# Optimization experiments

Measured on AMD Instinct MI355X. Metric: run time of the kernel, lower is better.

## Reference

```python
import jax, jax.numpy as jnp
import numpy as np

NUM_HEADS = 16
HEAD_DIM = 64
SCALE = HEAD_DIM ** -0.5


def setup_inputs() -> dict:
    key = jax.random.key(0)
    ks = jax.random.split(key, 5)
    B, N, C = 2, 2048, 1024
    x = jax.random.normal(ks[0], (B, N, C), dtype=jnp.float32)
    rel_pos_bias = jax.random.normal(ks[1], (NUM_HEADS, N, N), dtype=jnp.float32) * 0.02
    qkv_w = jax.random.normal(ks[2], (3 * C, C), dtype=jnp.float32) * (C ** -0.5)
    q_bias = jnp.zeros((C,), dtype=jnp.float32)
    v_bias = jnp.zeros((C,), dtype=jnp.float32)
    proj_w = jax.random.normal(ks[3], (C, C), dtype=jnp.float32) * (C ** -0.5)
    proj_b = jnp.zeros((C,), dtype=jnp.float32)
    return {"x": x, "rel_pos_bias": rel_pos_bias, "qkv_w": qkv_w,
            "q_bias": q_bias, "v_bias": v_bias, "proj_w": proj_w, "proj_b": proj_b}


def reference(x, rel_pos_bias, qkv_w, q_bias, v_bias, proj_w, proj_b):
    B, N, C = x.shape
    H, D = NUM_HEADS, HEAD_DIM
    # qkv bias = concat(q_bias, zeros, v_bias)
    qkv_b = jnp.concatenate([q_bias, jnp.zeros_like(v_bias), v_bias])
    qkv = x @ qkv_w.T + qkv_b                       # [B, N, 3C]
    qkv = qkv.reshape(B, N, 3, H, D).transpose(2, 0, 3, 1, 4)  # [3, B, H, N, D]
    q, k, v = qkv[0], qkv[1], qkv[2]
    q = q * SCALE
    attn = jnp.einsum('bhnd,bhmd->bhnm', q, k)      # [B, H, N, N]
    attn = attn + rel_pos_bias[None]                # bias broadcast over batch
    attn = jax.nn.softmax(attn, axis=-1)
    out = jnp.einsum('bhnm,bhmd->bhnd', attn, v)    # [B, H, N, D]
    out = out.transpose(0, 2, 1, 3).reshape(B, N, H * D)
    out = out @ proj_w.T + proj_b
    return out
```

## Files before the change

kernel.cpp:

```cpp
#include <hip/hip_runtime.h>

typedef unsigned short u16;
typedef short bfrag __attribute__((ext_vector_type(8)));
typedef float facc  __attribute__((ext_vector_type(4)));

#define LOG2E 1.44269504088896340736f

static __device__ __forceinline__ u16 f2bf(float x) {
  union { float f; unsigned u; } v; v.f = x;
  return (u16)((v.u + 0x7FFFu + ((v.u >> 16) & 1u)) >> 16);
}
static __device__ __forceinline__ void gload_lds16(const u16* g, u16* l) {
  __builtin_amdgcn_global_load_lds((const __attribute__((address_space(1))) void*)g,
                                   (__attribute__((address_space(3))) void*)l,
                                   16, 0, 0);
}
static __device__ __forceinline__ void gload_lds16f_nt(const float* g, float* l) {
  __builtin_amdgcn_global_load_lds((const __attribute__((address_space(1))) void*)g,
                                   (__attribute__((address_space(3))) void*)l,
                                   16, 0, 2);
}

__global__ __launch_bounds__(256) void convert_kernel(
    const float* __restrict__ x, const float* __restrict__ qw, const float* __restrict__ pw,
    u16* __restrict__ xb, u16* __restrict__ qwb, u16* __restrict__ pwb)
{
  const int NX = 4 * 1024 * 1024, NQ = 3 * 1024 * 1024, NP = 1024 * 1024;
  const int total4 = (NX + NQ + NP) >> 2;
  for (int i = blockIdx.x * blockDim.x + threadIdx.x; i < total4;
       i += gridDim.x * blockDim.x) {
    const int e = i << 2;
    const float* s; u16* d; int off;
    if (e < NX)            { s = x;  d = xb;  off = e; }
    else if (e < NX + NQ)  { s = qw; d = qwb; off = e - NX; }
    else                   { s = pw; d = pwb; off = e - NX - NQ; }
    float4 v = *(const float4*)(s + off);
    ushort4 o;
    o.x = f2bf(v.x); o.y = f2bf(v.y); o.z = f2bf(v.z); o.w = f2bf(v.w);
    *(ushort4*)(d + off) = o;
  }
}

static __device__ __forceinline__ void gemm128_bt(
    const u16* __restrict__ A, const u16* __restrict__ B, int K,
    int m0, int n0, u16* As, u16* Bs, facc acc[4][4])
{
  const int lane = threadIdx.x & 63;
  const int wv   = threadIdx.x >> 6;
  const int quad = lane >> 4;
  const int l15  = lane & 15;
  const int wm = wv >> 1, wn = wv & 1;
  const int srow = lane >> 2;
  const int skb  = (lane & 3) * 8;

  facc zero = {0.f, 0.f, 0.f, 0.f};
#pragma unroll
  for (int i = 0; i < 4; ++i)
#pragma unroll
    for (int j = 0; j < 4; ++j) acc[i][j] = zero;

  const int nIter = K >> 5;
  for (int kk = 0; kk < nIter; ++kk) {
    const int k0 = kk << 5;
    __syncthreads();
#pragma unroll
    for (int c = 0; c < 2; ++c) {
      const int seg = wv * 2 + c;
      gload_lds16(A + (long)(m0 + seg * 16 + srow) * K + k0 + skb, As + seg * 512);
      gload_lds16(B + (long)(n0 + seg * 16 + srow) * K + k0 + skb, Bs + seg * 512);
    }
    __syncthreads();
    bfrag af[4], bf[4];
#pragma unroll
    for (int i = 0; i < 4; ++i)
      af[i] = *(const bfrag*)(As + (wm * 64 + i * 16 + l15) * 32 + quad * 8);
#pragma unroll
    for (int j = 0; j < 4; ++j)
      bf[j] = *(const bfrag*)(Bs + (wn * 64 + j * 16 + l15) * 32 + quad * 8);
#pragma unroll
    for (int i = 0; i < 4; ++i)
#pragma unroll
      for (int j = 0; j < 4; ++j)
        acc[i][j] = __builtin_amdgcn_mfma_f32_16x16x32_bf16(af[i], bf[j], acc[i][j], 0, 0, 0);
  }
}

__global__ __launch_bounds__(256) void qkv_gemm_kernel(
    const u16* __restrict__ x, const u16* __restrict__ w,
    const float* __restrict__ qb, const float* __restrict__ vb,
    u16* __restrict__ Q, u16* __restrict__ Kd, u16* __restrict__ Vt)
{
  __shared__ u16 As[128 * 32];
  __shared__ u16 Bs[128 * 32];
  facc acc[4][4];
  const int m0 = blockIdx.y * 128;
  const int n0 = blockIdx.x * 128;
  gemm128_bt(x, w, 1024, m0, n0, As, Bs, acc);

  const int lane = threadIdx.x & 63;
  const int wv = threadIdx.x >> 6;
  const int quad = lane >> 4, l15 = lane & 15;
  const int wm = wv >> 1, wn = wv & 1;
  const int ncb = n0 + wn * 64;
  const int which = ncb >> 10;
  const int h = (ncb >> 6) & 15;

#pragma unroll
  for (int j = 0; j < 4; ++j) {
    const int d = j * 16 + l15;
    const int n_g = ncb + d;
#pragma unroll
    for (int i = 0; i < 4; ++i) {
      const int mg0 = m0 + wm * 64 + i * 16 + quad * 4;
      const int b  = mg0 >> 11;
      const int ns = mg0 & 2047;
      if (which == 0) {
        const float qbv = qb[n_g];
#pragma unroll
        for (int r = 0; r < 4; ++r)
          Q[(((long)(b * 16 + h) * 2048 + ns + r) << 6) + d] =
              f2bf((acc[i][j][r] + qbv) * 0.125f);
      } else if (which == 1) {
#pragma unroll
        for (int r = 0; r < 4; ++r)
          Kd[(((long)(b * 16 + h) * 2048 + ns + r) << 6) + d] = f2bf(acc[i][j][r]);
      } else {
        const float vbv = vb[n_g - 2048];
        ushort4 pk;
        pk.x = f2bf(acc[i][j][0] + vbv);
        pk.y = f2bf(acc[i][j][1] + vbv);
        pk.z = f2bf(acc[i][j][2] + vbv);
        pk.w = f2bf(acc[i][j][3] + vbv);
        *(ushort4*)(Vt + (((long)((b * 16 + h) * 64 + d)) << 11) + ns) = pk;
      }
    }
  }
}

__global__ __launch_bounds__(256, 8) void attn_kernel(
    const u16* __restrict__ Q, const u16* __restrict__ Kd, const u16* __restrict__ Vt,
    const float* __restrict__ bias, float* __restrict__ Part)
{
  __shared__ u16 P[4][16 * 64];
  __shared__ float BiasS[2][2][16 * 64];
  const int lane = threadIdx.x & 63;
  const int wv = threadIdx.x >> 6;
  const int quad = lane >> 4, l15 = lane & 15;
  const int L  = (blockIdx.x & 7) * 256 + (blockIdx.x >> 3);
  const int h  = L >> 7;
  const int ks = (L >> 6) & 1;
  const int qg = L & 63;
  const int q0 = qg * 32;
  const int b  = wv & 1;
  const int qh = wv >> 1;
  const int bh = b * 16 + h;
  const int qw = q0 + qh * 16;
  const int ksBase = ks << 10;
  const long baseN = (long)bh << 17;

  bfrag qf0 = *(const bfrag*)(Q + baseN + (long)(qw + l15) * 64 + quad * 8);
  bfrag qf1 = *(const bfrag*)(Q + baseN + (long)(qw + l15) * 64 + 32 + quad * 8);

  facc o[4];
  float m_i[4], l_i[4];
  facc zero = {0.f, 0.f, 0.f, 0.f};
#pragma unroll
  for (int t = 0; t < 4; ++t) o[t] = zero;
#pragma unroll
  for (int r = 0; r < 4; ++r) { m_i[r] = -1e30f; l_i[r] = 0.f; }

  const float* bh_bias = bias + ((long)h << 22) + ((long)q0 << 11);
  char* PwB = (char*)&P[wv][0];

  auto stage = [&](int buf, int kk) {
#pragma unroll
    for (int cc = 0; cc < 2; ++cc) {
      const int c_ = b * 2 + cc;
      const int row_ = c_ * 4 + quad;
      gload_lds16f_nt(bh_bias + (long)(qh * 16 + row_) * 2048 + kk
                        + ((l15 * 4) ^ ((row_ & 7) << 2)),
                      &BiasS[buf][qh][0] + c_ * 256);
    }
  };

  stage(0, ksBase);

  for (int it = 0; it < 16; ++it) {
    const int k0 = ksBase + it * 64;
    __syncthreads();

    facc s[4];
#pragma unroll
    for (int kt = 0; kt < 4; ++kt) {
      const u16* kb = Kd + baseN + (long)(k0 + kt * 16 + l15) * 64;
      bfrag kf0 = *(const bfrag*)(kb + quad * 8);
      bfrag kf1 = *(const bfrag*)(kb + 32 + quad * 8);
      facc z = zero;
      z = __builtin_amdgcn_mfma_f32_16x16x32_bf16(qf0, kf0, z, 0, 0, 0);
      z = __builtin_amdgcn_mfma_f32_16x16x32_bf16(qf1, kf1, z, 0, 0, 0);
      s[kt] = z;
    }

    const float* bs = &BiasS[it & 1][qh][0];
#pragma unroll
    for (int kt = 0; kt < 4; ++kt)
#pragma unroll
      for (int r = 0; r < 4; ++r) {
        const int row = quad * 4 + r;
        s[kt][r] += bs[row * 64 + ((kt * 16 + l15) ^ ((row & 7) << 2))];
      }

    if (it + 1 < 16) stage((it + 1) & 1, k0 + 64);

    float alpha[4];
#pragma unroll
    for (int r = 0; r < 4; ++r) {
      float v = fmaxf(fmaxf(s[0][r], s[1][r]), fmaxf(s[2][r], s[3][r]));
      v = fmaxf(v, __shfl_xor(v, 1, 16));
      v = fmaxf(v, __shfl_xor(v, 2, 16));
      v = fmaxf(v, __shfl_xor(v, 4, 16));
      v = fmaxf(v, __shfl_xor(v, 8, 16));
      const float mn = fmaxf(m_i[r], v);
      alpha[r] = exp2f((m_i[r] - mn) * LOG2E);
      m_i[r] = mn;
    }
#pragma unroll
    for (int r = 0; r < 4; ++r) {
      const float p0 = exp2f((s[0][r] - m_i[r]) * LOG2E);
      const float p1 = exp2f((s[1][r] - m_i[r]) * LOG2E);
      const float p2 = exp2f((s[2][r] - m_i[r]) * LOG2E);
      const float p3 = exp2f((s[3][r] - m_i[r]) * LOG2E);
      s[0][r] = p0; s[1][r] = p1; s[2][r] = p2; s[3][r] = p3;
      float v = (p0 + p1) + (p2 + p3);
      v += __shfl_xor(v, 1, 16);
      v += __shfl_xor(v, 2, 16);
      v += __shfl_xor(v, 4, 16);
      v += __shfl_xor(v, 8, 16);
      l_i[r] = l_i[r] * alpha[r] + v;
    }
#pragma unroll
    for (int t = 0; t < 4; ++t)
#pragma unroll
      for (int r = 0; r < 4; ++r) o[t][r] *= alpha[r];

#pragma unroll
    for (int kt = 0; kt < 4; ++kt)
#pragma unroll
      for (int r = 0; r < 4; ++r) {
        const int bo = (kt * 2 + (l15 >> 3)) * 256 + (quad * 4 + r) * 16 + (l15 & 7) * 2;
        *(u16*)(PwB + bo) = f2bf(s[kt][r]);
      }

#pragma unroll
    for (int p = 0; p < 2; ++p) {
      bfrag pfp = *(const bfrag*)(PwB + p * 1024 + lane * 16);
#pragma unroll
      for (int t = 0; t < 4; ++t) {
        bfrag vf = *(const bfrag*)(Vt + baseN + (((long)(t * 16 + l15)) << 11)
                                   + k0 + p * 32 + quad * 8);
        o[t] = __builtin_amdgcn_mfma_f32_16x16x32_bf16(pfp, vf, o[t], 0, 0, 0);
      }
    }
  }

  const long prBase = ((long)ks * 65536 + (long)bh * 2048 + qw) * 80;
#pragma unroll
  for (int t = 0; t < 4; ++t)
#pragma unroll
    for (int r = 0; r < 4; ++r)
      Part[prBase + (long)(quad * 4 + r) * 80 + t * 16 + l15] = o[t][r];
#pragma unroll
  for (int r = 0; r < 4; ++r)
    if (l15 < 2)
      Part[prBase + (long)(quad * 4 + r) * 80 + 64 + l15] = (l15 == 0) ? m_i[r] : l_i[r];
}

__global__ __launch_bounds__(256) void combine_kernel(
    const float* __restrict__ Part, u16* __restrict__ AO)
{
  const int lane = threadIdx.x & 63;
  const int wv = threadIdx.x >> 6;
  const long row = (long)blockIdx.x * 4 + wv;
  const int bh = (int)(row >> 11);
  const int q  = (int)(row & 2047);
  const int b = bh >> 4, h = bh & 15;
  const float* p0 = Part + row * 80;
  const float* p1 = Part + (row + 65536) * 80;
  const float o0 = p0[lane], o1 = p1[lane];
  const float m0 = p0[64], l0 = p0[65];
  const float m1 = p1[64], l1 = p1[65];
  const float m = fmaxf(m0, m1);
  const float w0 = exp2f((m0 - m) * LOG2E);
  const float w1 = exp2f((m1 - m) * LOG2E);
  const float ov = (o0 * w0 + o1 * w1) / (l0 * w0 + l1 * w1);
  AO[(((long)(b * 2048 + q)) << 10) + h * 64 + lane] = f2bf(ov);
}

__global__ __launch_bounds__(256) void proj_kernel(
    const u16* __restrict__ Ain, const u16* __restrict__ w,
    const float* __restrict__ pb, float* __restrict__ out)
{
  __shared__ u16 As[128 * 32];
  __shared__ u16 Bs[128 * 32];
  facc acc[4][4];
  const int m0 = blockIdx.y * 128;
  const int n0 = blockIdx.x * 128;
  gemm128_bt(Ain, w, 1024, m0, n0, As, Bs, acc);

  const int lane = threadIdx.x & 63;
  const int wv = threadIdx.x >> 6;
  const int quad = lane >> 4, l15 = lane & 15;
  const int wm = wv >> 1, wn = wv & 1;
#pragma unroll
  for (int j = 0; j < 4; ++j) {
    const int n_g = n0 + wn * 64 + j * 16 + l15;
    const float pbv = pb[n_g];
#pragma unroll
    for (int i = 0; i < 4; ++i) {
      const int mg0 = m0 + wm * 64 + i * 16 + quad * 4;
#pragma unroll
      for (int r = 0; r < 4; ++r)
        out[(((long)(mg0 + r)) << 10) + n_g] = acc[i][j][r] + pbv;
    }
  }
}

extern "C" void kernel_launch(void* const* d_in, const int* in_sizes, int n_in,
                              void* d_out, int out_size, void* d_ws, size_t ws_size,
                              hipStream_t stream)
{
  const float* x    = (const float*)d_in[0];
  const float* bias = (const float*)d_in[1];
  const float* qkvw = (const float*)d_in[2];
  const float* qb   = (const float*)d_in[3];
  const float* vb   = (const float*)d_in[4];
  const float* pw   = (const float*)d_in[5];
  const float* pb   = (const float*)d_in[6];
  float* out = (float*)d_out;

  char* ws = (char*)d_ws;
  u16* Q    = (u16*)(ws);
  u16* Kd   = (u16*)(ws + (size_t)8  * 1024 * 1024);
  u16* Vt   = (u16*)(ws + (size_t)16 * 1024 * 1024);
  u16* AO   = (u16*)(ws + (size_t)24 * 1024 * 1024);
  u16* xb   = (u16*)(ws + (size_t)32 * 1024 * 1024);
  u16* qwb  = (u16*)(ws + (size_t)40 * 1024 * 1024);
  u16* pwb  = (u16*)(ws + (size_t)46 * 1024 * 1024);
  float* Part = (float*)(ws + (size_t)48 * 1024 * 1024);

  hipLaunchKernelGGL(convert_kernel, dim3(1024), dim3(256), 0, stream,
                     x, qkvw, pw, xb, qwb, pwb);
  hipLaunchKernelGGL(qkv_gemm_kernel, dim3(24, 32), dim3(256), 0, stream,
                     xb, qwb, qb, vb, Q, Kd, Vt);
  hipLaunchKernelGGL(attn_kernel, dim3(2048), dim3(256), 0, stream,
                     Q, Kd, Vt, bias, Part);
  hipLaunchKernelGGL(combine_kernel, dim3(16384), dim3(256), 0, stream,
                     Part, AO);
  hipLaunchKernelGGL(proj_kernel, dim3(8, 32), dim3(256), 0, stream,
                     AO, pwb, pb, out);
}
```

Baseline: 656.8 us.

## Transpose MFMA operands so each lane owns one query row in attention

Swaps the A/B operands of the QK^T and PV MFMAs so the accumulator holds S^T/O^T, giving each lane a single query row. Row max and sum now need 2 cross-quad shuffles instead of 4 per row for 4 rows, and only one m/l scalar per lane. Bias reads, P stores and output stores become vectorized 16B/8B accesses with a matching swizzle. Launch bounds are relaxed from 8 to 6 waves per SIMD, which gives the compiler more registers but may lower occupancy.

```diff
diff --git a/kernel.cpp b/kernel.cpp
--- a/kernel.cpp
+++ b/kernel.cpp
@@ -137,7 +137,7 @@
   }
 }
 
-__global__ __launch_bounds__(256, 8) void attn_kernel(
+__global__ __launch_bounds__(256, 6) void attn_kernel(
     const u16* __restrict__ Q, const u16* __restrict__ Kd, const u16* __restrict__ Vt,
     const float* __restrict__ bias, float* __restrict__ Part)
 {
@@ -162,12 +162,10 @@
   bfrag qf1 = *(const bfrag*)(Q + baseN + (long)(qw + l15) * 64 + 32 + quad * 8);
 
   facc o[4];
-  float m_i[4], l_i[4];
+  float m_i = -1e30f, l_i = 0.f;
   facc zero = {0.f, 0.f, 0.f, 0.f};
 #pragma unroll
   for (int t = 0; t < 4; ++t) o[t] = zero;
-#pragma unroll
-  for (int r = 0; r < 4; ++r) { m_i[r] = -1e30f; l_i[r] = 0.f; }
 
   const float* bh_bias = bias + ((long)h << 22) + ((long)q0 << 11);
   char* PwB = (char*)&P[wv][0];
@@ -196,60 +194,60 @@
       bfrag kf0 = *(const bfrag*)(kb + quad * 8);
       bfrag kf1 = *(const bfrag*)(kb + 32 + quad * 8);
       facc z = zero;
-      z = __builtin_amdgcn_mfma_f32_16x16x32_bf16(qf0, kf0, z, 0, 0, 0);
-      z = __builtin_amdgcn_mfma_f32_16x16x32_bf16(qf1, kf1, z, 0, 0, 0);
+      z = __builtin_amdgcn_mfma_f32_16x16x32_bf16(kf0, qf0, z, 0, 0, 0);
+      z = __builtin_amdgcn_mfma_f32_16x16x32_bf16(kf1, qf1, z, 0, 0, 0);
       s[kt] = z;
     }
 
     const float* bs = &BiasS[it & 1][qh][0];
+    const int bswz = (l15 & 7) << 2;
+#pragma unroll
+    for (int kt = 0; kt < 4; ++kt) {
+      const facc bv = *(const facc*)(bs + l15 * 64 + ((kt * 16 + quad * 4) ^ bswz));
+#pragma unroll
+      for (int r = 0; r < 4; ++r) s[kt][r] += bv[r];
+    }
+
+    if (it + 1 < 16) stage((it + 1) & 1, k0 + 64);
+
+    float mk[4];
 #pragma unroll
     for (int kt = 0; kt < 4; ++kt)
-#pragma unroll
-      for (int r = 0; r < 4; ++r) {
-        const int row = quad * 4 + r;
-        s[kt][r] += bs[row * 64 + ((kt * 16 + l15) ^ ((row & 7) << 2))];
-      }
-
-    if (it + 1 < 16) stage((it + 1) & 1, k0 + 64);
-
-    float alpha[4];
-#pragma unroll
-    for (int r = 0; r < 4; ++r) {
-      float v = fmaxf(fmaxf(s[0][r], s[1][r]), fmaxf(s[2][r], s[3][r]));
-      v = fmaxf(v, __shfl_xor(v, 1, 16));
-      v = fmaxf(v, __shfl_xor(v, 2, 16));
-      v = fmaxf(v, __shfl_xor(v, 4, 16));
-      v = fmaxf(v, __shfl_xor(v, 8, 16));
-      const float mn = fmaxf(m_i[r], v);
-      alpha[r] = exp2f((m_i[r] - mn) * LOG2E);
-      m_i[r] = mn;
-    }
-#pragma unroll
-    for (int r = 0; r < 4; ++r) {
-      const float p0 = exp2f((s[0][r] - m_i[r]) * LOG2E);
-      const float p1 = exp2f((s[1][r] - m_i[r]) * LOG2E);
-      const float p2 = exp2f((s[2][r] - m_i[r]) * LOG2E);
-      const float p3 = exp2f((s[3][r] - m_i[r]) * LOG2E);
-      s[0][r] = p0; s[1][r] = p1; s[2][r] = p2; s[3][r] = p3;
-      float v = (p0 + p1) + (p2 + p3);
-      v += __shfl_xor(v, 1, 16);
-      v += __shfl_xor(v, 2, 16);
-      v += __shfl_xor(v, 4, 16);
-      v += __shfl_xor(v, 8, 16);
-      l_i[r] = l_i[r] * alpha[r] + v;
-    }
+      mk[kt] = fmaxf(fmaxf(s[kt][0], s[kt][1]), fmaxf(s[kt][2], s[kt][3]));
+    float mx = fmaxf(fmaxf(mk[0], mk[1]), fmaxf(mk[2], mk[3]));
+    mx = fmaxf(mx, __shfl_xor(mx, 16));
+    mx = fmaxf(mx, __shfl_xor(mx, 32));
+    const float mn = fmaxf(m_i, mx);
+    const float alpha = exp2f((m_i - mn) * LOG2E);
+    m_i = mn;
+
+    float sum = 0.f;
+#pragma unroll
+    for (int kt = 0; kt < 4; ++kt) {
+      const float p0 = exp2f((s[kt][0] - mn) * LOG2E);
+      const float p1 = exp2f((s[kt][1] - mn) * LOG2E);
+      const float p2 = exp2f((s[kt][2] - mn) * LOG2E);
+      const float p3 = exp2f((s[kt][3] - mn) * LOG2E);
+      s[kt][0] = p0; s[kt][1] = p1; s[kt][2] = p2; s[kt][3] = p3;
+      sum += (p0 + p1) + (p2 + p3);
+    }
+    sum += __shfl_xor(sum, 16);
+    sum += __shfl_xor(sum, 32);
+    l_i = l_i * alpha + sum;
 #pragma unroll
     for (int t = 0; t < 4; ++t)
 #pragma unroll
-      for (int r = 0; r < 4; ++r) o[t][r] *= alpha[r];
-
-#pragma unroll
-    for (int kt = 0; kt < 4; ++kt)
-#pragma unroll
-      for (int r = 0; r < 4; ++r) {
-        const int bo = (kt * 2 + (l15 >> 3)) * 256 + (quad * 4 + r) * 16 + (l15 & 7) * 2;
-        *(u16*)(PwB + bo) = f2bf(s[kt][r]);
-      }
+      for (int r = 0; r < 4; ++r) o[t][r] *= alpha;
+
+#pragma unroll
+    for (int kt = 0; kt < 4; ++kt) {
+      ushort4 pk;
+      pk.x = f2bf(s[kt][0]); pk.y = f2bf(s[kt][1]);
+      pk.z = f2bf(s[kt][2]); pk.w = f2bf(s[kt][3]);
+      const int bo = (kt >> 1) * 1024 + (((kt * 2) + (quad >> 1)) & 3) * 256
+                   + l15 * 16 + (quad & 1) * 8;
+      *(ushort4*)(PwB + bo) = pk;
+    }
 
 #pragma unroll
     for (int p = 0; p < 2; ++p) {
@@ -258,21 +256,20 @@
       for (int t = 0; t < 4; ++t) {
         bfrag vf = *(const bfrag*)(Vt + baseN + (((long)(t * 16 + l15)) << 11)
                                    + k0 + p * 32 + quad * 8);
-        o[t] = __builtin_amdgcn_mfma_f32_16x16x32_bf16(pfp, vf, o[t], 0, 0, 0);
+        o[t] = __builtin_amdgcn_mfma_f32_16x16x32_bf16(vf, pfp, o[t], 0, 0, 0);
       }
     }
   }
 
   const long prBase = ((long)ks * 65536 + (long)bh * 2048 + qw) * 80;
+  float* prow = Part + prBase + (long)l15 * 80;
 #pragma unroll
   for (int t = 0; t < 4; ++t)
-#pragma unroll
-    for (int r = 0; r < 4; ++r)
-      Part[prBase + (long)(quad * 4 + r) * 80 + t * 16 + l15] = o[t][r];
-#pragma unroll
-  for (int r = 0; r < 4; ++r)
-    if (l15 < 2)
-      Part[prBase + (long)(quad * 4 + r) * 80 + 64 + l15] = (l15 == 0) ? m_i[r] : l_i[r];
+    *(facc*)(prow + t * 16 + quad * 4) = o[t];
+  if (quad == 0) {
+    float2 ml; ml.x = m_i; ml.y = l_i;
+    *(float2*)(prow + 64) = ml;
+  }
 }
 
 __global__ __launch_bounds__(256) void combine_kernel(
```

After: 741.0 us. 1.13x slower.
